# Optimization experiments

Hardware: AMD Instinct MI355X
Metric: run time of the kernel (lower is better)

The kernel has to match this reference:

```python
import jax, jax.numpy as jnp
import numpy as np

N = 50000
E = 800000
IN_C = 128
HID = 128
OUT_C = 2


def _linear_params(key, fan_in, fan_out):
    k1, k2 = jax.random.split(key)
    bound = 1.0 / np.sqrt(fan_in)
    W = jax.random.uniform(k1, (fan_in, fan_out), jnp.float32, -bound, bound)
    b = jax.random.uniform(k2, (fan_out,), jnp.float32, -bound, bound)
    return W, b


def setup_inputs() -> dict:
    key = jax.random.key(0)
    ks = jax.random.split(key, 9)
    x = jax.random.normal(ks[0], (N, IN_C), jnp.float32)
    edge_index = jax.random.randint(ks[1], (2, E), 0, N, jnp.int64)
    W1a, b1a = _linear_params(ks[2], IN_C, HID)
    W1b, b1b = _linear_params(ks[3], HID, HID)
    W2a, b2a = _linear_params(ks[4], HID, HID)
    W2b, b2b = _linear_params(ks[5], HID, HID)
    Wfc, bfc = _linear_params(ks[6], HID, OUT_C)
    return {
        "x": x, "edge_index": edge_index,
        "W1a": W1a, "b1a": b1a, "W1b": W1b, "b1b": b1b,
        "W2a": W2a, "b2a": b2a, "W2b": W2b, "b2b": b2b,
        "Wfc": Wfc, "bfc": bfc,
    }


def _gin_conv(x, src, dst, Wa, ba, Wb, bb):
    # GINConv with eps=0: h = MLP(x + sum_{j in N(i)} x_j)
    agg = jax.ops.segment_sum(x[src], dst, num_segments=N)  # [N, d]
    h = x + agg
    h = jax.nn.relu(h @ Wa + ba)
    return h @ Wb + bb


def reference(x, edge_index, W1a, b1a, W1b, b1b, W2a, b2a, W2b, b2b, Wfc, bfc):
    src, dst = edge_index[0], edge_index[1]  # messages flow src -> dst
    h = _gin_conv(x, src, dst, W1a, b1a, W1b, b1b)
    h = jax.nn.relu(h)
    # dropout is identity in eval mode
    h = _gin_conv(h, src, dst, W2a, b2a, W2b, b2b)
    return h @ Wfc + bfc  # [N, 2]
```

## Files before the change

kernel.cpp:

```cpp
#include <hip/hip_runtime.h>

#define N_NODES 50000
#define N_EDGES 800000
#define NBUK    392
#define B_A     1024
#define EPB     782
#define CAPB    2560

typedef unsigned short u16;
typedef unsigned int   u32;
typedef __bf16 bf16x8 __attribute__((ext_vector_type(8)));
typedef float  f32x4  __attribute__((ext_vector_type(4)));

__device__ __forceinline__ float bf_lo(u32 v){ return __uint_as_float(v << 16); }
__device__ __forceinline__ float bf_hi(u32 v){ return __uint_as_float(v & 0xffff0000u); }
__device__ __forceinline__ u32 bf_pack(float a, float b){
    u32 ua = __float_as_uint(a), ub = __float_as_uint(b);
    ua += 0x7fffu + ((ua >> 16) & 1u);
    ub += 0x7fffu + ((ub >> 16) & 1u);
    return (ua >> 16) | (ub & 0xffff0000u);
}
__device__ __forceinline__ u16 f2bf(float a){
    u32 ua = __float_as_uint(a);
    ua += 0x7fffu + ((ua >> 16) & 1u);
    return (u16)(ua >> 16);
}
__device__ __forceinline__ void addu4(uint4 v, float* a){
    a[0] += bf_lo(v.x); a[1] += bf_hi(v.x);
    a[2] += bf_lo(v.y); a[3] += bf_hi(v.y);
    a[4] += bf_lo(v.z); a[5] += bf_hi(v.z);
    a[6] += bf_lo(v.w); a[7] += bf_hi(v.w);
}

__device__ __forceinline__ int blockScan256(int v, int* ws, int t) {
    int lane = t & 63, w = t >> 6;
    #pragma unroll
    for (int off = 1; off < 64; off <<= 1) {
        int u = __shfl_up(v, off);
        if (lane >= off) v += u;
    }
    if (lane == 63) ws[w] = v;
    __syncthreads();
    int add = 0;
    for (int k = 0; k < w; k++) add += ws[k];
    return v + add;
}

__device__ __forceinline__ int blockScan512(int v, int* ws, int t) {
    int lane = t & 63, w = t >> 6;
    #pragma unroll
    for (int off = 1; off < 64; off <<= 1) {
        int u = __shfl_up(v, off);
        if (lane >= off) v += u;
    }
    if (lane == 63) ws[w] = v;
    __syncthreads();
    int add = 0;
    for (int k = 0; k < w; k++) add += ws[k];
    return v + add;
}

__launch_bounds__(256)
__global__ void binA_kernel(const int* __restrict__ esrc, const int* __restrict__ edst,
                            u32* __restrict__ binned, int* __restrict__ startTab,
                            int* __restrict__ cntTab,
                            const float* __restrict__ xsrc, u32* __restrict__ xb,
                            const float* __restrict__ W1a, const float* __restrict__ W1b,
                            const float* __restrict__ W2a, const float* __restrict__ W2b,
                            const float* __restrict__ Wfc, const float* __restrict__ b2b,
                            const float* __restrict__ bfc,
                            u16* __restrict__ wt1a, u16* __restrict__ wt1b,
                            u16* __restrict__ wt2a,
                            float* __restrict__ Wc, float* __restrict__ bc) {
    int t = threadIdx.x, blk = blockIdx.x;
    if (blk >= B_A) {
        int b = blk - B_A;
        if (b < 192) {
            int g  = b * 256 + t;
            int mi = g >> 14;
            int p  = g & 16383;
            int k  = p >> 7, m = p & 127;
            const float* src = (mi == 0) ? W1a : (mi == 1) ? W1b : W2a;
            u16* dst         = (mi == 0) ? wt1a : (mi == 1) ? wt1b : wt2a;
            dst[m * 128 + k] = f2bf(src[k * 128 + m]);
        } else {
            int j = t >> 1, o = t & 1;
            float s = 0.f;
            for (int k = 0; k < 128; k++)
                s += W2b[j * 128 + k] * Wfc[k * 2 + o];
            Wc[j * 2 + o] = s;
            if (t < 2) {
                float s2 = 0.f;
                for (int k = 0; k < 128; k++)
                    s2 += b2b[k] * Wfc[k * 2 + t];
                bc[t] = s2 + bfc[t];
            }
        }
        return;
    }
    __shared__ int hist[NBUK];
    __shared__ int cur[NBUK];
    __shared__ u32 ebuf[EPB];
    __shared__ int ws[4];
    int base = blk * EPB;
    for (int i = t; i < NBUK; i += 256) hist[i] = 0;
    __syncthreads();
    for (int i = t; i < EPB; i += 256) {
        int gi = base + i;
        if (gi < N_EDGES) atomicAdd(&hist[edst[gi] >> 7], 1);
    }
    __syncthreads();
    int c0 = 0, c1 = 0;
    if (t < 196) { c0 = hist[2 * t]; c1 = hist[2 * t + 1]; }
    int s2 = c0 + c1;
    int incl = blockScan256(s2, ws, t);
    int excl = incl - s2;
    if (t < 196) {
        startTab[(2 * t) * B_A + blk]     = excl;
        cntTab[(2 * t) * B_A + blk]       = c0;
        cur[2 * t] = excl;
        startTab[(2 * t + 1) * B_A + blk] = excl + c0;
        cntTab[(2 * t + 1) * B_A + blk]   = c1;
        cur[2 * t + 1] = excl + c0;
    }
    __syncthreads();
    for (int i = t; i < EPB; i += 256) {
        int gi = base + i;
        if (gi < N_EDGES) {
            int d = edst[gi], s = esrc[gi];
            int p = atomicAdd(&cur[d >> 7], 1);
            ebuf[p] = (u32)s | ((u32)(d & 127) << 16);
        }
    }
    __syncthreads();
    for (int i = t; i < EPB; i += 256)
        binned[base + i] = ebuf[i];
    const int total = N_NODES * 64;
    for (int i = blk * 256 + t; i < total; i += B_A * 256) {
        float2 f = ((const float2*)xsrc)[i];
        xb[i] = bf_pack(f.x, f.y);
    }
}

__launch_bounds__(512, 4)
__global__ void bconv1_kernel(const u32* __restrict__ binned,
                              const int* __restrict__ startTab, const int* __restrict__ cntTab,
                              const u32* __restrict__ xb,
                              const u16* __restrict__ WA, const float* __restrict__ bA,
                              const u16* __restrict__ WB, const float* __restrict__ bB,
                              int2* __restrict__ span, int* __restrict__ csr,
                              u16* __restrict__ h1, int n) {
    __shared__ __align__(16) char shbuf[34816 + 10240 + 512 + 512 + 32 + 16];
    u16 (*As)[136] = (u16(*)[136])shbuf;
    u32* ebuf      = (u32*)shbuf;
    int* cbuf      = (int*)(shbuf + 34816);
    int* hist      = (int*)(shbuf + 34816 + 10240);
    int* cursor    = (int*)(shbuf + 34816 + 10240 + 512);
    int* ws        = (int*)(shbuf + 34816 + 10240 + 1024);
    int* totsh     = ws + 8;
    int b = blockIdx.x, t = threadIdx.x;

    int c2[2], rs2[2], s = 0;
    #pragma unroll
    for (int q = 0; q < 2; q++) {
        int run = t * 2 + q;
        c2[q]  = cntTab[b * B_A + run];
        rs2[q] = run * EPB + startTab[b * B_A + run];
        s += c2[q];
    }
    int incl = blockScan512(s, ws, t);
    int rb = incl - s;
    if (t == 511) *totsh = incl;
    if (t < 128) hist[t] = 0;
    __syncthreads();
    #pragma unroll
    for (int q = 0; q < 2; q++) {
        int c = c2[q], rs = rs2[q];
        for (int k = 0; k < c; k++) {
            int p = rb + k;
            if (p < CAPB) ebuf[p] = binned[rs + k];
        }
        rb += c;
    }
    __syncthreads();
    int tot = *totsh;
    if (tot > CAPB) tot = CAPB;
    for (int i = t; i < tot; i += 512)
        atomicAdd(&hist[ebuf[i] >> 16], 1);
    __syncthreads();
    int hv = (t < 128) ? hist[t] : 0;
    int hincl = blockScan512(hv, ws, t);
    int hexcl = hincl - hv;
    int gb = b * CAPB;
    if (t < 128) {
        hist[t]   = hexcl;
        cursor[t] = hexcl;
        int node = (b << 7) + t;
        if (node < n) span[node] = make_int2(gb + hexcl, gb + hexcl + hv);
    }
    __syncthreads();
    for (int i = t; i < tot; i += 512) {
        u32 e = ebuf[i];
        int p = atomicAdd(&cursor[e >> 16], 1);
        cbuf[p] = (int)(e & 0xFFFFu);
    }
    __syncthreads();
    for (int i = t; i < tot; i += 512)
        csr[gb + i] = cbuf[i];
    __syncthreads();

    int row0 = b * 128;
    int w = t >> 6, lane = t & 63;
    int g4 = lane >> 4, l16 = lane & 15;
    const uint4* xp = (const uint4*)xb;
    #pragma unroll
    for (int p = 0; p < 4; p++) {
        int rl = w * 16 + p * 4 + g4;
        int node = row0 + rl;
        float a[8] = {0.f,0.f,0.f,0.f,0.f,0.f,0.f,0.f};
        if (node < n) {
            addu4(xp[(size_t)node * 16 + l16], a);
            int j = hist[rl], jend = cursor[rl];
            for (; j + 8 <= jend; j += 8) {
                int s0 = cbuf[j],     s1 = cbuf[j + 1], s2b = cbuf[j + 2], s3 = cbuf[j + 3];
                int s4 = cbuf[j + 4], s5 = cbuf[j + 5], s6 = cbuf[j + 6], s7 = cbuf[j + 7];
                uint4 v0 = xp[(size_t)s0 * 16 + l16], v1 = xp[(size_t)s1 * 16 + l16];
                uint4 v2 = xp[(size_t)s2b * 16 + l16], v3 = xp[(size_t)s3 * 16 + l16];
                uint4 v4 = xp[(size_t)s4 * 16 + l16], v5 = xp[(size_t)s5 * 16 + l16];
                uint4 v6 = xp[(size_t)s6 * 16 + l16], v7 = xp[(size_t)s7 * 16 + l16];
                addu4(v0, a); addu4(v1, a); addu4(v2, a); addu4(v3, a);
                addu4(v4, a); addu4(v5, a); addu4(v6, a); addu4(v7, a);
            }
            for (; j + 4 <= jend; j += 4) {
                int s0 = cbuf[j], s1 = cbuf[j + 1], s2b = cbuf[j + 2], s3 = cbuf[j + 3];
                uint4 v0 = xp[(size_t)s0 * 16 + l16], v1 = xp[(size_t)s1 * 16 + l16];
                uint4 v2 = xp[(size_t)s2b * 16 + l16], v3 = xp[(size_t)s3 * 16 + l16];
                addu4(v0, a); addu4(v1, a); addu4(v2, a); addu4(v3, a);
            }
            for (; j < jend; j++)
                addu4(xp[(size_t)cbuf[j] * 16 + l16], a);
        }
        uint4 pk = make_uint4(bf_pack(a[0], a[1]), bf_pack(a[2], a[3]),
                              bf_pack(a[4], a[5]), bf_pack(a[6], a[7]));
        *(uint4*)&As[rl][l16 * 8] = pk;
    }
    int lm = l16, lq = g4;
    f32x4 acc[8];
    #pragma unroll
    for (int c = 0; c < 8; c++) acc[c] = (f32x4){0.f, 0.f, 0.f, 0.f};
    #pragma unroll
    for (int kk = 0; kk < 4; kk++) {
        bf16x8 af = *(const bf16x8*)&As[w * 16 + lm][kk * 32 + lq * 8];
        #pragma unroll
        for (int c = 0; c < 8; c++) {
            bf16x8 bf = *(const bf16x8*)(WA + (size_t)(c * 16 + lm) * 128 + kk * 32 + lq * 8);
            acc[c] = __builtin_amdgcn_mfma_f32_16x16x32_bf16(af, bf, acc[c], 0, 0, 0);
        }
    }
    #pragma unroll
    for (int c = 0; c < 8; c++) {
        int col = c * 16 + lm;
        float bcol = bA[col];
        #pragma unroll
        for (int r = 0; r < 4; r++) {
            float v = acc[c][r] + bcol;
            v = v > 0.f ? v : 0.f;
            As[w * 16 + lq * 4 + r][col] = f2bf(v);
        }
    }
    f32x4 acc2[8];
    #pragma unroll
    for (int c = 0; c < 8; c++) acc2[c] = (f32x4){0.f, 0.f, 0.f, 0.f};
    #pragma unroll
    for (int kk = 0; kk < 4; kk++) {
        bf16x8 af = *(const bf16x8*)&As[w * 16 + lm][kk * 32 + lq * 8];
        #pragma unroll
        for (int c = 0; c < 8; c++) {
            bf16x8 bf = *(const bf16x8*)(WB + (size_t)(c * 16 + lm) * 128 + kk * 32 + lq * 8);
            acc2[c] = __builtin_amdgcn_mfma_f32_16x16x32_bf16(af, bf, acc2[c], 0, 0, 0);
        }
    }
    #pragma unroll
    for (int c = 0; c < 8; c++) {
        int col = c * 16 + lm;
        float bcol = bB[col];
        #pragma unroll
        for (int r = 0; r < 4; r++) {
            int row = row0 + w * 16 + lq * 4 + r;
            if (row < n) {
                float v = acc2[c][r] + bcol;
                v = v > 0.f ? v : 0.f;
                h1[(size_t)row * 128 + col] = f2bf(v);
            }
        }
    }
}

__launch_bounds__(256, 4)
__global__ void fconv2_kernel(const u32* __restrict__ xb,
                              const u16* __restrict__ WA, const float* __restrict__ bA,
                              const float* __restrict__ Wc, const float* __restrict__ bc,
                              const int2* __restrict__ span, const int* __restrict__ csr,
                              float2* __restrict__ out, int n) {
    __shared__ u16 As[64][136];
    int t = threadIdx.x;
    int row0 = blockIdx.x * 64;
    int w = t >> 6, lane = t & 63;
    int g4 = lane >> 4, l16 = lane & 15;
    const uint4* xp = (const uint4*)xb;
    #pragma unroll
    for (int p = 0; p < 4; p++) {
        int rl = w * 16 + p * 4 + g4;
        int node = row0 + rl;
        float a[8] = {0.f,0.f,0.f,0.f,0.f,0.f,0.f,0.f};
        if (node < n) {
            addu4(xp[(size_t)node * 16 + l16], a);
            int2 sp = span[node];
            int j = sp.x, jend = sp.y;
            for (; j + 8 <= jend; j += 8) {
                int s0 = csr[j],     s1 = csr[j + 1], s2 = csr[j + 2], s3 = csr[j + 3];
                int s4 = csr[j + 4], s5 = csr[j + 5], s6 = csr[j + 6], s7 = csr[j + 7];
                uint4 v0 = xp[(size_t)s0 * 16 + l16], v1 = xp[(size_t)s1 * 16 + l16];
                uint4 v2 = xp[(size_t)s2 * 16 + l16], v3 = xp[(size_t)s3 * 16 + l16];
                uint4 v4 = xp[(size_t)s4 * 16 + l16], v5 = xp[(size_t)s5 * 16 + l16];
                uint4 v6 = xp[(size_t)s6 * 16 + l16], v7 = xp[(size_t)s7 * 16 + l16];
                addu4(v0, a); addu4(v1, a); addu4(v2, a); addu4(v3, a);
                addu4(v4, a); addu4(v5, a); addu4(v6, a); addu4(v7, a);
            }
            for (; j + 4 <= jend; j += 4) {
                int s0 = csr[j], s1 = csr[j + 1], s2 = csr[j + 2], s3 = csr[j + 3];
                uint4 v0 = xp[(size_t)s0 * 16 + l16], v1 = xp[(size_t)s1 * 16 + l16];
                uint4 v2 = xp[(size_t)s2 * 16 + l16], v3 = xp[(size_t)s3 * 16 + l16];
                addu4(v0, a); addu4(v1, a); addu4(v2, a); addu4(v3, a);
            }
            for (; j < jend; j++)
                addu4(xp[(size_t)csr[j] * 16 + l16], a);
        }
        uint4 pk = make_uint4(bf_pack(a[0], a[1]), bf_pack(a[2], a[3]),
                              bf_pack(a[4], a[5]), bf_pack(a[6], a[7]));
        *(uint4*)&As[rl][l16 * 8] = pk;
    }
    int lm = l16, lq = g4;
    f32x4 acc[8];
    #pragma unroll
    for (int c = 0; c < 8; c++) acc[c] = (f32x4){0.f, 0.f, 0.f, 0.f};
    #pragma unroll
    for (int kk = 0; kk < 4; kk++) {
        bf16x8 af = *(const bf16x8*)&As[w * 16 + lm][kk * 32 + lq * 8];
        #pragma unroll
        for (int c = 0; c < 8; c++) {
            bf16x8 bf = *(const bf16x8*)(WA + (size_t)(c * 16 + lm) * 128 + kk * 32 + lq * 8);
            acc[c] = __builtin_amdgcn_mfma_f32_16x16x32_bf16(af, bf, acc[c], 0, 0, 0);
        }
    }
    float p0[4] = {0,0,0,0}, p1[4] = {0,0,0,0};
    #pragma unroll
    for (int c = 0; c < 8; c++) {
        int col = c * 16 + lm;
        float bcol = bA[col];
        float2 wc = ((const float2*)Wc)[col];
        #pragma unroll
        for (int r = 0; r < 4; r++) {
            float v = acc[c][r] + bcol;
            v = v > 0.f ? v : 0.f;
            p0[r] += v * wc.x;
            p1[r] += v * wc.y;
        }
    }
    #pragma unroll
    for (int off = 1; off < 16; off <<= 1) {
        #pragma unroll
        for (int r = 0; r < 4; r++) {
            p0[r] += __shfl_xor(p0[r], off);
            p1[r] += __shfl_xor(p1[r], off);
        }
    }
    if (lm == 0) {
        float b0 = bc[0], b1 = bc[1];
        #pragma unroll
        for (int r = 0; r < 4; r++) {
            int row = row0 + w * 16 + lq * 4 + r;
            if (row < n) out[row] = make_float2(p0[r] + b0, p1[r] + b1);
        }
    }
}

extern "C" void kernel_launch(void* const* d_in, const int* in_sizes, int n_in,
                              void* d_out, int out_size, void* d_ws, size_t ws_size,
                              hipStream_t stream) {
    const float* x   = (const float*)d_in[0];
    const int*   ei  = (const int*)d_in[1];
    const float* W1a = (const float*)d_in[2];
    const float* b1a = (const float*)d_in[3];
    const float* W1b = (const float*)d_in[4];
    const float* b1b = (const float*)d_in[5];
    const float* W2a = (const float*)d_in[6];
    const float* b2a = (const float*)d_in[7];
    const float* W2b = (const float*)d_in[8];
    const float* b2b = (const float*)d_in[9];
    const float* Wfc = (const float*)d_in[10];
    const float* bfc = (const float*)d_in[11];

    const int* esrc = ei;
    const int* edst = ei + N_EDGES;

    char* w = (char*)d_ws;
    size_t off = 0;
    auto alloc = [&](size_t bytes) -> char* {
        char* p = w + off;
        off = (off + bytes + 255) & ~(size_t)255;
        return p;
    };
    int2*  span       = (int2*)alloc((size_t)N_NODES * 8);
    int*   startTab   = (int*)alloc((size_t)NBUK * B_A * 4);
    int*   cntTab     = (int*)alloc((size_t)NBUK * B_A * 4);
    int*   csr        = (int*)alloc((size_t)NBUK * CAPB * 4);
    u32*   binned     = (u32*)alloc((size_t)B_A * EPB * 4);
    u16*   wt1a       = (u16*)alloc(128 * 128 * 2);
    u16*   wt1b       = (u16*)alloc(128 * 128 * 2);
    u16*   wt2a       = (u16*)alloc(128 * 128 * 2);
    float* Wc         = (float*)alloc(256 * 4);
    float* bc         = (float*)alloc(2 * 4);
    u16*   bufA       = (u16*)alloc((size_t)N_NODES * 128 * 2);
    u16*   bufB       = (u16*)alloc((size_t)N_NODES * 128 * 2);

    binA_kernel<<<B_A + 193, 256, 0, stream>>>(esrc, edst, binned, startTab, cntTab,
                                               x, (u32*)bufB,
                                               W1a, W1b, W2a, W2b, Wfc, b2b, bfc,
                                               wt1a, wt1b, wt2a, Wc, bc);
    bconv1_kernel<<<NBUK, 512, 0, stream>>>(binned, startTab, cntTab,
                                            (const u32*)bufB, wt1a, b1a, wt1b, b1b,
                                            span, csr, bufA, N_NODES);
    fconv2_kernel<<<(N_NODES + 63) / 64, 256, 0, stream>>>((const u32*)bufA, wt2a, b2a,
                                                           Wc, bc, span, csr,
                                                           (float2*)d_out, N_NODES);
}
```

Measured before the change: 211.1 us.

## Bin edges into per-bucket global buffers via atomic reservations

Binning now uses 128 large blocks that each reserve space in a per-bucket global buffer with one atomicAdd per bucket. The next stage then reads each bucket as a contiguous segment and no longer scans 1024 per-block start and count tables. The x-to-bf16 conversion moves into its own set of blocks so it no longer sits behind binning. The cost is fewer binning blocks, each with a larger shared buffer, plus an extra memset. Edge order inside a bucket now depends on atomic ordering, which is nondeterministic.

```diff
diff --git a/kernel.cpp b/kernel.cpp
--- a/kernel.cpp
+++ b/kernel.cpp
@@ -3,8 +3,9 @@
 #define N_NODES 50000
 #define N_EDGES 800000
 #define NBUK    392
-#define B_A     1024
-#define EPB     782
+#define B_BIN   128
+#define EPB     6250
+#define NCVT    1024
 #define CAPB    2560
 
 typedef unsigned short u16;
@@ -62,8 +63,7 @@
 
 __launch_bounds__(256)
 __global__ void binA_kernel(const int* __restrict__ esrc, const int* __restrict__ edst,
-                            u32* __restrict__ binned, int* __restrict__ startTab,
-                            int* __restrict__ cntTab,
+                            u32* __restrict__ bukBuf, int* __restrict__ bukCnt,
                             const float* __restrict__ xsrc, u32* __restrict__ xb,
                             const float* __restrict__ W1a, const float* __restrict__ W1b,
                             const float* __restrict__ W2a, const float* __restrict__ W2b,
@@ -73,17 +73,24 @@
                             u16* __restrict__ wt2a,
                             float* __restrict__ Wc, float* __restrict__ bc) {
     int t = threadIdx.x, blk = blockIdx.x;
-    if (blk >= B_A) {
-        int b = blk - B_A;
-        if (b < 192) {
-            int g  = b * 256 + t;
+    __shared__ u32 ebuf[EPB];
+    __shared__ int hist[NBUK];
+    __shared__ int cur[NBUK];
+    __shared__ int gbase[NBUK];
+    __shared__ int ws[4];
+    if (blk >= B_BIN) {
+        int pb = blk - B_BIN;
+        if (pb < 192) {
+            int g  = pb * 256 + t;
             int mi = g >> 14;
             int p  = g & 16383;
             int k  = p >> 7, m = p & 127;
             const float* src = (mi == 0) ? W1a : (mi == 1) ? W1b : W2a;
             u16* dst         = (mi == 0) ? wt1a : (mi == 1) ? wt1b : wt2a;
             dst[m * 128 + k] = f2bf(src[k * 128 + m]);
-        } else {
+            return;
+        }
+        if (pb == 192) {
             int j = t >> 1, o = t & 1;
             float s = 0.f;
             for (int k = 0; k < 128; k++)
@@ -95,20 +102,21 @@
                     s2 += b2b[k] * Wfc[k * 2 + t];
                 bc[t] = s2 + bfc[t];
             }
+            return;
+        }
+        int cb = pb - 193;
+        const int total = N_NODES * 64;
+        for (int i = cb * 256 + t; i < total; i += NCVT * 256) {
+            float2 f = ((const float2*)xsrc)[i];
+            xb[i] = bf_pack(f.x, f.y);
         }
         return;
     }
-    __shared__ int hist[NBUK];
-    __shared__ int cur[NBUK];
-    __shared__ u32 ebuf[EPB];
-    __shared__ int ws[4];
     int base = blk * EPB;
     for (int i = t; i < NBUK; i += 256) hist[i] = 0;
     __syncthreads();
-    for (int i = t; i < EPB; i += 256) {
-        int gi = base + i;
-        if (gi < N_EDGES) atomicAdd(&hist[edst[gi] >> 7], 1);
-    }
+    for (int i = t; i < EPB; i += 256)
+        atomicAdd(&hist[edst[base + i] >> 7], 1);
     __syncthreads();
     int c0 = 0, c1 = 0;
     if (t < 196) { c0 = hist[2 * t]; c1 = hist[2 * t + 1]; }
@@ -116,35 +124,35 @@
     int incl = blockScan256(s2, ws, t);
     int excl = incl - s2;
     if (t < 196) {
-        startTab[(2 * t) * B_A + blk]     = excl;
-        cntTab[(2 * t) * B_A + blk]       = c0;
-        cur[2 * t] = excl;
-        startTab[(2 * t + 1) * B_A + blk] = excl + c0;
-        cntTab[(2 * t + 1) * B_A + blk]   = c1;
-        cur[2 * t + 1] = excl + c0;
+        hist[2 * t]     = excl;          cur[2 * t]     = excl;
+        hist[2 * t + 1] = excl + c0;     cur[2 * t + 1] = excl + c0;
     }
     __syncthreads();
     for (int i = t; i < EPB; i += 256) {
         int gi = base + i;
-        if (gi < N_EDGES) {
-            int d = edst[gi], s = esrc[gi];
-            int p = atomicAdd(&cur[d >> 7], 1);
-            ebuf[p] = (u32)s | ((u32)(d & 127) << 16);
-        }
-    }
-    __syncthreads();
-    for (int i = t; i < EPB; i += 256)
-        binned[base + i] = ebuf[i];
-    const int total = N_NODES * 64;
-    for (int i = blk * 256 + t; i < total; i += B_A * 256) {
-        float2 f = ((const float2*)xsrc)[i];
-        xb[i] = bf_pack(f.x, f.y);
+        int d = edst[gi], s = esrc[gi];
+        u32 e = (u32)s | ((u32)(d & 127) << 16) | ((u32)(d >> 7) << 23);
+        int p = atomicAdd(&cur[d >> 7], 1);
+        ebuf[p] = e;
+    }
+    __syncthreads();
+    for (int j = t; j < NBUK; j += 256) {
+        int cnt = cur[j] - hist[j];
+        gbase[j] = cnt ? atomicAdd(&bukCnt[j], cnt) : 0;
+    }
+    __syncthreads();
+    for (int i = t; i < EPB; i += 256) {
+        u32 e = ebuf[i];
+        int b9 = (int)(e >> 23);
+        u32 idx = (u32)(gbase[b9] + (i - hist[b9]));
+        if (idx < CAPB)
+            bukBuf[(size_t)b9 * CAPB + idx] = e;
     }
 }
 
 __launch_bounds__(512, 4)
-__global__ void bconv1_kernel(const u32* __restrict__ binned,
-                              const int* __restrict__ startTab, const int* __restrict__ cntTab,
+__global__ void bconv1_kernel(const u32* __restrict__ bukBuf,
+                              const int* __restrict__ bukCnt,
                               const u32* __restrict__ xb,
                               const u16* __restrict__ WA, const float* __restrict__ bA,
                               const u16* __restrict__ WB, const float* __restrict__ bB,
@@ -157,36 +165,17 @@
     int* hist      = (int*)(shbuf + 34816 + 10240);
     int* cursor    = (int*)(shbuf + 34816 + 10240 + 512);
     int* ws        = (int*)(shbuf + 34816 + 10240 + 1024);
-    int* totsh     = ws + 8;
     int b = blockIdx.x, t = threadIdx.x;
 
-    int c2[2], rs2[2], s = 0;
-    #pragma unroll
-    for (int q = 0; q < 2; q++) {
-        int run = t * 2 + q;
-        c2[q]  = cntTab[b * B_A + run];
-        rs2[q] = run * EPB + startTab[b * B_A + run];
-        s += c2[q];
-    }
-    int incl = blockScan512(s, ws, t);
-    int rb = incl - s;
-    if (t == 511) *totsh = incl;
+    int tot = bukCnt[b];
+    if (tot > CAPB) tot = CAPB;
     if (t < 128) hist[t] = 0;
     __syncthreads();
-    #pragma unroll
-    for (int q = 0; q < 2; q++) {
-        int c = c2[q], rs = rs2[q];
-        for (int k = 0; k < c; k++) {
-            int p = rb + k;
-            if (p < CAPB) ebuf[p] = binned[rs + k];
-        }
-        rb += c;
-    }
-    __syncthreads();
-    int tot = *totsh;
-    if (tot > CAPB) tot = CAPB;
-    for (int i = t; i < tot; i += 512)
-        atomicAdd(&hist[ebuf[i] >> 16], 1);
+    for (int i = t; i < tot; i += 512) {
+        u32 e = bukBuf[(size_t)b * CAPB + i];
+        ebuf[i] = e;
+        atomicAdd(&hist[(e >> 16) & 127], 1);
+    }
     __syncthreads();
     int hv = (t < 128) ? hist[t] : 0;
     int hincl = blockScan512(hv, ws, t);
@@ -201,7 +190,7 @@
     __syncthreads();
     for (int i = t; i < tot; i += 512) {
         u32 e = ebuf[i];
-        int p = atomicAdd(&cursor[e >> 16], 1);
+        int p = atomicAdd(&cursor[(e >> 16) & 127], 1);
         cbuf[p] = (int)(e & 0xFFFFu);
     }
     __syncthreads();
@@ -412,10 +401,9 @@
         return p;
     };
     int2*  span       = (int2*)alloc((size_t)N_NODES * 8);
-    int*   startTab   = (int*)alloc((size_t)NBUK * B_A * 4);
-    int*   cntTab     = (int*)alloc((size_t)NBUK * B_A * 4);
     int*   csr        = (int*)alloc((size_t)NBUK * CAPB * 4);
-    u32*   binned     = (u32*)alloc((size_t)B_A * EPB * 4);
+    u32*   bukBuf     = (u32*)alloc((size_t)NBUK * CAPB * 4);
+    int*   bukCnt     = (int*)alloc((size_t)NBUK * 4);
     u16*   wt1a       = (u16*)alloc(128 * 128 * 2);
     u16*   wt1b       = (u16*)alloc(128 * 128 * 2);
     u16*   wt2a       = (u16*)alloc(128 * 128 * 2);
@@ -424,11 +412,12 @@
     u16*   bufA       = (u16*)alloc((size_t)N_NODES * 128 * 2);
     u16*   bufB       = (u16*)alloc((size_t)N_NODES * 128 * 2);
 
-    binA_kernel<<<B_A + 193, 256, 0, stream>>>(esrc, edst, binned, startTab, cntTab,
-                                               x, (u32*)bufB,
-                                               W1a, W1b, W2a, W2b, Wfc, b2b, bfc,
-                                               wt1a, wt1b, wt2a, Wc, bc);
-    bconv1_kernel<<<NBUK, 512, 0, stream>>>(binned, startTab, cntTab,
+    hipMemsetAsync(bukCnt, 0, (size_t)NBUK * 4, stream);
+    binA_kernel<<<B_BIN + 193 + NCVT, 256, 0, stream>>>(esrc, edst, bukBuf, bukCnt,
+                                                        x, (u32*)bufB,
+                                                        W1a, W1b, W2a, W2b, Wfc, b2b, bfc,
+                                                        wt1a, wt1b, wt2a, Wc, bc);
+    bconv1_kernel<<<NBUK, 512, 0, stream>>>(bukBuf, bukCnt,
                                             (const u32*)bufB, wt1a, b1a, wt1b, b1b,
                                             span, csr, bufA, N_NODES);
     fconv2_kernel<<<(N_NODES + 63) / 64, 256, 0, stream>>>((const u32*)bufA, wt2a, b2a,
```

After: 213.0 us. Within noise of the previous version (+0.9%).
